# Performance work log

Hardware: AMD Instinct MI355X
Metric: run time of the kernel (lower is better)

## Reference

```python
import jax, jax.numpy as jnp
import numpy as np

B, S, D, H = 16, 512, 768, 12
DH = D // H


def setup_inputs() -> dict:
    key = jax.random.key(0)
    ks = jax.random.split(key, 12)
    hidden_states = jax.random.normal(ks[0], (B, S, D), dtype=jnp.float32)
    # additive padding mask: 0 for valid, -10000 for padded tail tokens
    lengths = jax.random.randint(ks[1], (B,), S // 2, S + 1)
    pad = (jnp.arange(S)[None, :] >= lengths[:, None]).astype(jnp.float32)
    attention_mask = (pad * -10000.0)[:, None, None, :]  # [B,1,1,S]
    # row-stochastic graph prior over codes
    pr = jax.random.uniform(ks[2], (B, S, S), dtype=jnp.float32)
    prior = pr / jnp.sum(pr, axis=-1, keepdims=True)
    s = 0.02
    params = dict(
        Wq=jax.random.normal(ks[3], (D, D)) * s, bq=jnp.zeros((D,)),
        Wk=jax.random.normal(ks[4], (D, D)) * s, bk=jnp.zeros((D,)),
        Wv=jax.random.normal(ks[5], (D, D)) * s, bv=jnp.zeros((D,)),
        Wg=jax.random.normal(ks[6], (D, 2)) * s, bg=jnp.zeros((2,)),
        Wo=jax.random.normal(ks[7], (D, D)) * s, bo=jnp.zeros((D,)),
        gamma=jnp.ones((D,)), beta=jnp.zeros((D,)),
    )
    return dict(hidden_states=hidden_states, attention_mask=attention_mask,
                prior=prior, **params)


def _layer_norm(x, gamma, beta, eps=1e-5):
    mu = jnp.mean(x, axis=-1, keepdims=True)
    var = jnp.mean(jnp.square(x - mu), axis=-1, keepdims=True)
    return (x - mu) * jax.lax.rsqrt(var + eps) * gamma + beta


def reference(hidden_states, attention_mask, prior,
              Wq, bq, Wk, bk, Wv, bv, Wg, bg, Wo, bo, gamma, beta):
    b, s, d = hidden_states.shape
    # project and split heads: [B,S,H,DH]
    q = (hidden_states @ Wq + bq).reshape(b, s, H, DH)
    k = (hidden_states @ Wk + bk).reshape(b, s, H, DH)
    v = (hidden_states @ Wv + bv).reshape(b, s, H, DH)
    scores = jnp.einsum('bshd,bthd->bhst', q, k) / jnp.sqrt(jnp.float32(DH))
    scores = scores + attention_mask  # broadcast [B,1,1,S]
    probs = jax.nn.softmax(scores, axis=-1)  # [B,H,S,S]
    # gate: avg-pool over valid tokens, softmax(linear/2)
    valid = (attention_mask.squeeze((1, 2)) == 0.0).astype(hidden_states.dtype)  # [B,S]
    denom = jnp.maximum(jnp.sum(valid, axis=1, keepdims=True), 1.0)
    h_pool = jnp.sum(hidden_states * valid[:, :, None], axis=1) / denom  # [B,D]
    gate = jax.nn.softmax((h_pool @ Wg + bg) / 2.0, axis=-1)  # [B,2]
    probs = probs * gate[:, 0, None, None, None] + prior[:, None, :, :] * gate[:, 1, None, None, None]
    ctx = jnp.einsum('bhst,bthd->bshd', probs, v).reshape(b, s, d)
    out = jax.nn.relu(ctx @ Wo + bo)
    out = _layer_norm(out + hidden_states, gamma, beta)
    return out
```

## Files before the change

kernel.cpp:

```cpp
#include <hip/hip_runtime.h>

#define NB_ 16
#define S_ 512
#define D_ 768
#define H_ 12
#define DH_ 64
#define QT_ 64
#define KT_ 128
#define LDQ_ 1536

typedef __attribute__((ext_vector_type(8))) short bf16x8;
typedef __attribute__((ext_vector_type(4))) float f32x4;
typedef unsigned short ushort_t;

__device__ __forceinline__ unsigned short f2bf(float f){
  unsigned int u = __float_as_uint(f);
  u += 0x7fffu + ((u >> 16) & 1u);
  return (unsigned short)(u >> 16);
}
__device__ __forceinline__ float bf2f(unsigned short s){
  return __uint_as_float(((unsigned int)s) << 16);
}
__device__ __forceinline__ unsigned int pack2(float a, float b){
  return (unsigned int)f2bf(a) | ((unsigned int)f2bf(b) << 16);
}
__device__ __forceinline__ void gld16(const ushort_t* g, ushort_t* l){
  __builtin_amdgcn_global_load_lds((const __attribute__((address_space(1))) unsigned int*)g,
                                   (__attribute__((address_space(3))) unsigned int*)l, 16, 0, 0);
}

__global__ __launch_bounds__(256) void k_setup(
    const float* __restrict__ hs, const float* __restrict__ mask, const float* __restrict__ prior,
    const float* __restrict__ W0, const float* __restrict__ W1,
    const float* __restrict__ W2, const float* __restrict__ W3,
    const float* __restrict__ b0, const float* __restrict__ b1, const float* __restrict__ b2,
    ushort_t* __restrict__ hsb, ushort_t* __restrict__ wt, float* __restrict__ bqkv,
    float* __restrict__ partial, float* __restrict__ pcnt, ushort_t* __restrict__ priorb)
{
  __shared__ float t[32][33];
  const int bx = blockIdx.x, tid = threadIdx.x;
  if (bx < 512){
    int chunk = bx & 31, b = bx >> 5;
    const float* mrow = mask + b * S_ + chunk * 16;
    const float* base = hs + ((size_t)b * S_ + chunk * 16) * D_;
    ushort_t* obase = hsb + ((size_t)b * S_ + chunk * 16) * D_;
    float a0 = 0.f, a1 = 0.f, a2 = 0.f, cnt = 0.f;
#pragma unroll 2
    for (int s = 0; s < 16; s++){
      const float* r = base + (size_t)s * D_;
      float x0 = r[tid], x1 = r[tid + 256], x2 = r[tid + 512];
      ushort_t* o = obase + (size_t)s * D_;
      o[tid] = f2bf(x0); o[tid + 256] = f2bf(x1); o[tid + 512] = f2bf(x2);
      if (mrow[s] == 0.0f){ a0 += x0; a1 += x1; a2 += x2; cnt += 1.0f; }
    }
    float* o = partial + (size_t)(b * 32 + chunk) * D_;
    o[tid] = a0; o[tid + 256] = a1; o[tid + 512] = a2;
    if (tid == 0) pcnt[b * 32 + chunk] = cnt;
  } else if (bx < 512 + 2304){
    int idx = bx - 512;
    int z = idx / 576, rem = idx - z * 576;
    int ky = rem / 24, nx = rem - ky * 24;
    const float* W = (z == 0) ? W0 : (z == 1) ? W1 : (z == 2) ? W2 : W3;
    ushort_t* o = wt + (size_t)z * D_ * D_;
    int j = tid & 31, i0 = tid >> 5;
    int kb = ky * 32, nb = nx * 32;
#pragma unroll
    for (int r = 0; r < 4; r++){
      int i = i0 + r * 8;
      t[i][j] = W[(size_t)(kb + i) * D_ + nb + j];
    }
    __syncthreads();
#pragma unroll
    for (int r = 0; r < 4; r++){
      int i = i0 + r * 8;
      o[(size_t)(nb + i) * D_ + kb + j] = f2bf(t[j][i]);
    }
  } else if (bx < 2825){
    int i = (bx - 2816) * 256 + tid;
    if (i < 3 * D_){
      float v = (i < D_) ? b0[i] : (i < 2 * D_) ? b1[i - D_] : b2[i - 2 * D_];
      bqkv[i] = v;
    }
  } else {
    size_t i = (size_t)(bx - 2825) * 4096 + (size_t)tid * 16;
    const float4* s4 = (const float4*)(prior + i);
    float4 f0 = s4[0], f1 = s4[1], f2 = s4[2], f3 = s4[3];
    uint4 p0, p1;
    p0.x = pack2(f0.x, f0.y); p0.y = pack2(f0.z, f0.w);
    p0.z = pack2(f1.x, f1.y); p0.w = pack2(f1.z, f1.w);
    p1.x = pack2(f2.x, f2.y); p1.y = pack2(f2.z, f2.w);
    p1.z = pack2(f3.x, f3.y); p1.w = pack2(f3.z, f3.w);
    *(uint4*)(priorb + i) = p0;
    *(uint4*)(priorb + i + 8) = p1;
  }
}

__global__ __launch_bounds__(256) void k_pool2(const float* __restrict__ partial, const float* __restrict__ pcnt,
                                               const float* __restrict__ Wg, const float* __restrict__ bg,
                                               float* __restrict__ gate){
  int b = blockIdx.x, tid = threadIdx.x;
  __shared__ float red[256];
  __shared__ float hp[768];
  float a0 = 0.f, a1 = 0.f, a2 = 0.f;
#pragma unroll
  for (int c = 0; c < 32; c++){
    const float* p = partial + (size_t)(b * 32 + c) * D_;
    a0 += p[tid]; a1 += p[tid + 256]; a2 += p[tid + 512];
  }
  float denom = 0.f;
#pragma unroll
  for (int c = 0; c < 32; c++) denom += pcnt[b * 32 + c];
  float inv = 1.0f / fmaxf(denom, 1.0f);
  hp[tid] = a0 * inv; hp[tid + 256] = a1 * inv; hp[tid + 512] = a2 * inv;
  __syncthreads();
  float p0 = 0.f, p1 = 0.f;
  for (int d = tid; d < D_; d += 256){ p0 += hp[d] * Wg[d * 2]; p1 += hp[d] * Wg[d * 2 + 1]; }
  red[tid] = p0; __syncthreads();
  for (int o = 128; o > 0; o >>= 1){ if (tid < o) red[tid] += red[tid + o]; __syncthreads(); }
  float z0 = red[0]; __syncthreads();
  red[tid] = p1; __syncthreads();
  for (int o = 128; o > 0; o >>= 1){ if (tid < o) red[tid] += red[tid + o]; __syncthreads(); }
  float z1 = red[0];
  if (tid == 0){
    z0 = (z0 + bg[0]) * 0.5f; z1 = (z1 + bg[1]) * 0.5f;
    float m = fmaxf(z0, z1);
    float e0 = __expf(z0 - m), e1 = __expf(z1 - m);
    float ssum = e0 + e1;
    gate[b * 2] = e0 / ssum; gate[b * 2 + 1] = e1 / ssum;
  }
}

template<int OUTBF16, int RELU, int RESID, int MAP, int VSPLIT>
__global__ __launch_bounds__(256, 2) void k_gemm_bt(
    const ushort_t* __restrict__ Am, long sA, int lda,
    const ushort_t* __restrict__ Bm, long sB, int ldb,
    void* __restrict__ Cp, long sC, int ldc, void* __restrict__ Cp2,
    const float* __restrict__ bias,
    const float* __restrict__ resid, float alpha, int K)
{
  __shared__ ushort_t As[2][128 * 64];
  __shared__ ushort_t Bs[2][128 * 64];
  int z, bm, bn;
  if (MAP == 2){ z = blockIdx.x; bm = blockIdx.y; bn = blockIdx.z; }
  else if (MAP == 1){ z = blockIdx.z; bm = blockIdx.x; bn = blockIdx.y; }
  else { z = blockIdx.z; bm = blockIdx.y; bn = blockIdx.x; }
  const ushort_t* Ab = Am + (size_t)z * sA;
  const ushort_t* Bb = Bm + (size_t)z * sB;
  const long coff = (long)z * sC;
  const int tid = threadIdx.x;
  const int m0 = bm * 128, n0 = bn * 128;
  const int wid = tid >> 6, lane = tid & 63;
  const int quad = lane >> 4, l16 = lane & 15;
  const int wm = wid >> 1, wn = wid & 1;
  const int sw = l16 & 7;

  auto stage = [&](int buf, int k0){
#pragma unroll
    for (int c = 0; c < 4; c++){
      int idx = tid + c * 256;
      int row = idx >> 3, p = idx & 7;
      int cg = p ^ (row & 7);
      gld16(Ab + (size_t)(m0 + row) * lda + k0 + cg * 8, &As[buf][idx * 8]);
    }
#pragma unroll
    for (int c = 0; c < 4; c++){
      int idx = tid + c * 256;
      int row = idx >> 3, p = idx & 7;
      int cg = p ^ (row & 7);
      gld16(Bb + (size_t)(n0 + row) * ldb + k0 + cg * 8, &Bs[buf][idx * 8]);
    }
  };

  f32x4 acc[4][4];
#pragma unroll
  for (int i = 0; i < 4; i++)
#pragma unroll
    for (int j = 0; j < 4; j++) acc[i][j] = (f32x4){0.f, 0.f, 0.f, 0.f};

  stage(0, 0);
  int cur = 0;
  for (int k0 = 0; k0 < K; k0 += 64){
    if (k0 + 64 < K){
      stage(cur ^ 1, k0 + 64);
      __builtin_amdgcn_sched_barrier(0);
      asm volatile("s_waitcnt vmcnt(8)" ::: "memory");
    } else {
      __builtin_amdgcn_sched_barrier(0);
      asm volatile("s_waitcnt vmcnt(0)" ::: "memory");
    }
    __builtin_amdgcn_sched_barrier(0);
    __builtin_amdgcn_s_barrier();
#pragma unroll
    for (int ks = 0; ks < 2; ks++){
      bf16x8 af[4], bfv[4];
#pragma unroll
      for (int mi = 0; mi < 4; mi++){
        int row = wm * 64 + mi * 16 + l16;
        af[mi] = *(const bf16x8*)(&As[cur][(row * 8 + ((ks * 4 + quad) ^ sw)) * 8]);
      }
#pragma unroll
      for (int ni = 0; ni < 4; ni++){
        int row = wn * 64 + ni * 16 + l16;
        bfv[ni] = *(const bf16x8*)(&Bs[cur][(row * 8 + ((ks * 4 + quad) ^ sw)) * 8]);
      }
      __builtin_amdgcn_s_setprio(1);
#pragma unroll
      for (int mi = 0; mi < 4; mi++)
#pragma unroll
        for (int ni = 0; ni < 4; ni++)
          acc[mi][ni] = __builtin_amdgcn_mfma_f32_16x16x32_bf16(af[mi], bfv[ni], acc[mi][ni], 0, 0, 0);
      __builtin_amdgcn_s_setprio(0);
    }
    __builtin_amdgcn_sched_barrier(0);
    __builtin_amdgcn_s_barrier();
    cur ^= 1;
  }

  if (VSPLIT && n0 >= 1536){
    ushort_t* vtp = (ushort_t*)Cp2;
    const int bb = m0 >> 9;
#pragma unroll
    for (int mi = 0; mi < 4; mi++){
#pragma unroll
      for (int ni = 0; ni < 4; ni++){
        int col = n0 + wn * 64 + ni * 16 + l16;
        float bcol = bias[col];
        int hh = (col - 1536) >> 6, dh = (col - 1536) & 63;
        int trow = (m0 & 511) + wm * 64 + mi * 16 + quad * 4;
        uint2 pk;
        pk.x = pack2(acc[mi][ni][0] + bcol, acc[mi][ni][1] + bcol);
        pk.y = pack2(acc[mi][ni][2] + bcol, acc[mi][ni][3] + bcol);
        *(uint2*)(vtp + ((size_t)(bb * H_ + hh) * DH_ + dh) * S_ + trow) = pk;
      }
    }
    return;
  }

#pragma unroll
  for (int mi = 0; mi < 4; mi++){
#pragma unroll
    for (int ni = 0; ni < 4; ni++){
      int col = n0 + wn * 64 + ni * 16 + l16;
      float bcol = bias ? bias[col] : 0.0f;
#pragma unroll
      for (int r = 0; r < 4; r++){
        int row = m0 + wm * 64 + mi * 16 + quad * 4 + r;
        float v = acc[mi][ni][r] * alpha + bcol;
        if (RELU) v = fmaxf(v, 0.0f);
        if (RESID) v += resid[(size_t)row * ldc + col];
        long idx = coff + (long)row * ldc + col;
        if (OUTBF16) ((ushort_t*)Cp)[idx] = f2bf(v);
        else         ((float*)Cp)[idx] = v;
      }
    }
  }
}

__global__ __launch_bounds__(512, 2) void k_gemm8_qkv(
    const ushort_t* __restrict__ A,
    const ushort_t* __restrict__ B,
    ushort_t* __restrict__ Cq,
    ushort_t* __restrict__ vt,
    const float* __restrict__ bias)
{
  __shared__ ushort_t Al[2][2][256 * 32];
  __shared__ ushort_t Bl[2][2][256 * 32];
  const int tid = threadIdx.x;
  const int m0 = blockIdx.x * 256, n0 = blockIdx.y * 256;
  const int wid = tid >> 6, lane = tid & 63;
  const int quad = lane >> 4, l16 = lane & 15;
  const int wm = wid >> 2, wn = wid & 3;

  const int i0c = tid, i1c = tid + 512;
  const int r0 = i0c >> 2, c0 = (i0c & 3) ^ (r0 & 3);
  const int r1 = i1c >> 2, c1 = (i1c & 3) ^ (r1 & 3);
  const size_t a0 = (size_t)(m0 + r0) * 768 + c0 * 8;
  const size_t a1 = (size_t)(m0 + r1) * 768 + c1 * 8;
  const size_t b0 = (size_t)(n0 + r0) * 768 + c0 * 8;
  const size_t b1 = (size_t)(n0 + r1) * 768 + c1 * 8;

  auto stA = [&](int slot, int ks, int kt){
    int ko = kt * 64 + ks * 32;
    gld16(A + a0 + ko, &Al[slot][ks][i0c * 8]);
    gld16(A + a1 + ko, &Al[slot][ks][i1c * 8]);
  };
  auto stB = [&](int slot, int ks, int kt){
    int ko = kt * 64 + ks * 32;
    gld16(B + b0 + ko, &Bl[slot][ks][i0c * 8]);
    gld16(B + b1 + ko, &Bl[slot][ks][i1c * 8]);
  };
  auto rdA = [&](int slot, int ks, int mi) -> bf16x8 {
    int row = wm * 128 + mi * 16 + l16;
    return *(const bf16x8*)(&Al[slot][ks][(row * 4 + (quad ^ (row & 3))) * 8]);
  };
  auto rdB = [&](int slot, int ks, int ni) -> bf16x8 {
    int row = wn * 64 + ni * 16 + l16;
    return *(const bf16x8*)(&Bl[slot][ks][(row * 4 + (quad ^ (row & 3))) * 8]);
  };

  f32x4 acc[8][4];
#pragma unroll
  for (int i = 0; i < 8; i++)
#pragma unroll
    for (int j = 0; j < 4; j++) acc[i][j] = (f32x4){0.f, 0.f, 0.f, 0.f};

  stA(0, 0, 0); stB(0, 0, 0); stA(0, 1, 0); stB(0, 1, 0);
  stA(1, 0, 1); stB(1, 0, 1); stA(1, 1, 1);
  __builtin_amdgcn_sched_barrier(0);
  asm volatile("s_waitcnt vmcnt(6)" ::: "memory");
  __builtin_amdgcn_sched_barrier(0);
  __builtin_amdgcn_s_barrier();

#pragma unroll 2
  for (int t = 0; t < 12; ++t){
    const int s = t & 1, o = s ^ 1;
    bf16x8 aL[8], aH[8], bL[4], bH[4];
#pragma unroll
    for (int mi = 0; mi < 8; mi++) aL[mi] = rdA(s, 0, mi);
#pragma unroll
    for (int ni = 0; ni < 4; ni++) bL[ni] = rdB(s, 0, ni);
    if (t + 1 < 12) stB(o, 1, t + 1);
    __builtin_amdgcn_sched_barrier(0);
    __builtin_amdgcn_s_barrier();
    asm volatile("s_waitcnt lgkmcnt(0)" ::: "memory");
    __builtin_amdgcn_sched_barrier(0);
    __builtin_amdgcn_s_setprio(1);
#pragma unroll
    for (int mi = 0; mi < 4; mi++)
#pragma unroll
      for (int ni = 0; ni < 4; ni++)
        acc[mi][ni] = __builtin_amdgcn_mfma_f32_16x16x32_bf16(aL[mi], bL[ni], acc[mi][ni], 0, 0, 0);
    __builtin_amdgcn_s_setprio(0);
    __builtin_amdgcn_sched_barrier(0);
    __builtin_amdgcn_s_barrier();
#pragma unroll
    for (int ni = 0; ni < 4; ni++) bH[ni] = rdB(s, 1, ni);
    if (t + 2 < 12) stA(s, 0, t + 2);
    __builtin_amdgcn_sched_barrier(0);
    __builtin_amdgcn_s_barrier();
    asm volatile("s_waitcnt lgkmcnt(0)" ::: "memory");
    __builtin_amdgcn_sched_barrier(0);
    __builtin_amdgcn_s_setprio(1);
#pragma unroll
    for (int mi = 4; mi < 8; mi++)
#pragma unroll
      for (int ni = 0; ni < 4; ni++)
        acc[mi][ni] = __builtin_amdgcn_mfma_f32_16x16x32_bf16(aL[mi], bL[ni], acc[mi][ni], 0, 0, 0);
    __builtin_amdgcn_s_setprio(0);
    __builtin_amdgcn_sched_barrier(0);
    __builtin_amdgcn_s_barrier();
#pragma unroll
    for (int mi = 0; mi < 8; mi++) aH[mi] = rdA(s, 1, mi);
    if (t + 2 < 12) stB(s, 0, t + 2);
    __builtin_amdgcn_sched_barrier(0);
    __builtin_amdgcn_s_barrier();
    asm volatile("s_waitcnt lgkmcnt(0)" ::: "memory");
    __builtin_amdgcn_sched_barrier(0);
    __builtin_amdgcn_s_setprio(1);
#pragma unroll
    for (int mi = 0; mi < 4; mi++)
#pragma unroll
      for (int ni = 0; ni < 4; ni++)
        acc[mi][ni] = __builtin_amdgcn_mfma_f32_16x16x32_bf16(aH[mi], bH[ni], acc[mi][ni], 0, 0, 0);
    __builtin_amdgcn_s_setprio(0);
    __builtin_amdgcn_sched_barrier(0);
    __builtin_amdgcn_s_barrier();
    if (t + 2 < 12) stA(s, 1, t + 2);
    __builtin_amdgcn_sched_barrier(0);
    __builtin_amdgcn_s_barrier();
    __builtin_amdgcn_s_setprio(1);
#pragma unroll
    for (int mi = 4; mi < 8; mi++)
#pragma unroll
      for (int ni = 0; ni < 4; ni++)
        acc[mi][ni] = __builtin_amdgcn_mfma_f32_16x16x32_bf16(aH[mi], bH[ni], acc[mi][ni], 0, 0, 0);
    __builtin_amdgcn_s_setprio(0);
    __builtin_amdgcn_sched_barrier(0);
    if (t < 10) { asm volatile("s_waitcnt vmcnt(6)" ::: "memory"); }
    else        { asm volatile("s_waitcnt vmcnt(0)" ::: "memory"); }
    __builtin_amdgcn_sched_barrier(0);
    __builtin_amdgcn_s_barrier();
  }

  if (n0 >= 1536){
    const int bb = m0 >> 9;
#pragma unroll
    for (int mi = 0; mi < 8; mi++){
#pragma unroll
      for (int ni = 0; ni < 4; ni++){
        int col = n0 + wn * 64 + ni * 16 + l16;
        float bcol = bias[col];
        int hh = (col - 1536) >> 6, dh = (col - 1536) & 63;
        int trow = (m0 & 511) + wm * 128 + mi * 16 + quad * 4;
        uint2 pk;
        pk.x = pack2(acc[mi][ni][0] + bcol, acc[mi][ni][1] + bcol);
        pk.y = pack2(acc[mi][ni][2] + bcol, acc[mi][ni][3] + bcol);
        *(uint2*)(vt + ((size_t)(bb * H_ + hh) * DH_ + dh) * S_ + trow) = pk;
      }
    }
    return;
  }
#pragma unroll
  for (int mi = 0; mi < 8; mi++){
#pragma unroll
    for (int ni = 0; ni < 4; ni++){
      int col = n0 + wn * 64 + ni * 16 + l16;
      float bcol = bias[col];
#pragma unroll
      for (int r = 0; r < 4; r++){
        int row = m0 + wm * 128 + mi * 16 + quad * 4 + r;
        Cq[(size_t)row * LDQ_ + col] = f2bf(acc[mi][ni][r] + bcol);
      }
    }
  }
}

__global__ __launch_bounds__(256) void k_flash(
    const ushort_t* __restrict__ qkv,
    const ushort_t* __restrict__ vt,
    const ushort_t* __restrict__ priorctx,
    const float* __restrict__ mask,
    const float* __restrict__ gate,
    ushort_t* __restrict__ ctx)
{
  __shared__ ushort_t Ks[KT_ * 64];
  __shared__ ushort_t Vs[DH_ * 128];
  __shared__ ushort_t Ps[QT_ * 136];
  __shared__ float rs[QT_];
  const int z = blockIdx.x, b = z / H_, h = z - b * H_;
  const int q0 = blockIdx.y * QT_;
  const int tid = threadIdx.x;
  const int wid = tid >> 6, lane = tid & 63, quad = lane >> 4, l16 = lane & 15;

  bf16x8 bq[4][2];
#pragma unroll
  for (int ni = 0; ni < 4; ni++)
#pragma unroll
    for (int ks = 0; ks < 2; ks++)
      bq[ni][ks] = *(const bf16x8*)(qkv + ((size_t)(b * S_ + q0 + ni * 16 + l16)) * LDQ_
                                    + h * DH_ + ks * 32 + quad * 8);
  if (tid < QT_) rs[tid] = 0.f;

  f32x4 accv[4];
#pragma unroll
  for (int ni = 0; ni < 4; ni++) accv[ni] = (f32x4){0.f, 0.f, 0.f, 0.f};

  for (int t0 = 0; t0 < S_; t0 += KT_){
    if (mask[b * S_ + t0] != 0.0f) break;
#pragma unroll
    for (int c = 0; c < 4; c++){
      int idx = tid + c * 256;
      int row = idx >> 3, p = idx & 7;
      int cg = p ^ (row & 7);
      gld16(qkv + ((size_t)(b * S_ + t0 + row)) * LDQ_ + D_ + h * DH_ + cg * 8, &Ks[idx * 8]);
    }
#pragma unroll
    for (int c = 0; c < 4; c++){
      int idx = tid + c * 256;
      int row = idx >> 4, p = idx & 15;
      int cg = p ^ (row & 15);
      gld16(vt + (size_t)z * (DH_ * S_) + (size_t)row * S_ + t0 + cg * 8, &Vs[idx * 8]);
    }
    __syncthreads();

    f32x4 accs[2][4];
#pragma unroll
    for (int mi = 0; mi < 2; mi++)
#pragma unroll
      for (int ni = 0; ni < 4; ni++) accs[mi][ni] = (f32x4){0.f, 0.f, 0.f, 0.f};
#pragma unroll
    for (int ks = 0; ks < 2; ks++){
      bf16x8 ak[2];
#pragma unroll
      for (int mi = 0; mi < 2; mi++){
        int row = wid * 32 + mi * 16 + l16;
        ak[mi] = *(const bf16x8*)(&Ks[(row * 8 + ((ks * 4 + quad) ^ (l16 & 7))) * 8]);
      }
#pragma unroll
      for (int mi = 0; mi < 2; mi++)
#pragma unroll
        for (int ni = 0; ni < 4; ni++)
          accs[mi][ni] = __builtin_amdgcn_mfma_f32_16x16x32_bf16(ak[mi], bq[ni][ks], accs[mi][ni], 0, 0, 0);
    }

    float mv[2][4];
#pragma unroll
    for (int mi = 0; mi < 2; mi++)
#pragma unroll
      for (int r = 0; r < 4; r++)
        mv[mi][r] = mask[b * S_ + t0 + wid * 32 + mi * 16 + quad * 4 + r];
    float rowpart[4] = {0.f, 0.f, 0.f, 0.f};
#pragma unroll
    for (int mi = 0; mi < 2; mi++){
#pragma unroll
      for (int ni = 0; ni < 4; ni++){
        float e0 = __expf(accs[mi][ni][0] * 0.125f + mv[mi][0]);
        float e1 = __expf(accs[mi][ni][1] * 0.125f + mv[mi][1]);
        float e2 = __expf(accs[mi][ni][2] * 0.125f + mv[mi][2]);
        float e3 = __expf(accs[mi][ni][3] * 0.125f + mv[mi][3]);
        rowpart[ni] += (e0 + e1) + (e2 + e3);
        uint2 pk;
        pk.x = pack2(e0, e1);
        pk.y = pack2(e2, e3);
        *(uint2*)(&Ps[(ni * 16 + l16) * 136 + wid * 32 + mi * 16 + quad * 4]) = pk;
      }
    }
#pragma unroll
    for (int ni = 0; ni < 4; ni++){
      rowpart[ni] += __shfl_xor(rowpart[ni], 16);
      rowpart[ni] += __shfl_xor(rowpart[ni], 32);
    }
    if (lane < 16){
#pragma unroll
      for (int ni = 0; ni < 4; ni++) atomicAdd(&rs[ni * 16 + l16], rowpart[ni]);
    }
    __syncthreads();

#pragma unroll
    for (int ks = 0; ks < 4; ks++){
      bf16x8 ap = *(const bf16x8*)(&Ps[(wid * 16 + l16) * 136 + ks * 32 + quad * 8]);
#pragma unroll
      for (int ni = 0; ni < 4; ni++){
        bf16x8 bv8 = *(const bf16x8*)(&Vs[((ni * 16 + l16) * 16 + ((ks * 4 + quad) ^ l16)) * 8]);
        accv[ni] = __builtin_amdgcn_mfma_f32_16x16x32_bf16(ap, bv8, accv[ni], 0, 0, 0);
      }
    }
    __syncthreads();
  }

  const float g0 = gate[b * 2], g1 = gate[b * 2 + 1];
#pragma unroll
  for (int ni = 0; ni < 4; ni++){
#pragma unroll
    for (int r = 0; r < 4; r++){
      int q = wid * 16 + quad * 4 + r;
      int dh = ni * 16 + l16;
      float scl = g0 / rs[q];
      size_t idx = ((size_t)(b * S_ + q0 + q)) * D_ + h * DH_ + dh;
      float v = accv[ni][r] * scl + g1 * bf2f(priorctx[idx]);
      ctx[idx] = f2bf(v);
    }
  }
}

__global__ __launch_bounds__(256) void k_ln(float* __restrict__ out, const float* __restrict__ gamma,
                                            const float* __restrict__ beta){
  __shared__ float red[256];
  int row = blockIdx.x, tid = threadIdx.x;
  float* p = out + (size_t)row * D_;
  float x0 = p[tid], x1 = p[tid + 256], x2 = p[tid + 512];
  red[tid] = x0 + x1 + x2; __syncthreads();
  for (int o = 128; o > 0; o >>= 1){ if (tid < o) red[tid] += red[tid + o]; __syncthreads(); }
  float mu = red[0] * (1.0f / 768.0f);
  __syncthreads();
  float d0 = x0 - mu, d1 = x1 - mu, d2 = x2 - mu;
  red[tid] = d0 * d0 + d1 * d1 + d2 * d2; __syncthreads();
  for (int o = 128; o > 0; o >>= 1){ if (tid < o) red[tid] += red[tid + o]; __syncthreads(); }
  float rsv = rsqrtf(red[0] * (1.0f / 768.0f) + 1e-5f);
  p[tid]       = d0 * rsv * gamma[tid]       + beta[tid];
  p[tid + 256] = d1 * rsv * gamma[tid + 256] + beta[tid + 256];
  p[tid + 512] = d2 * rsv * gamma[tid + 512] + beta[tid + 512];
}

extern "C" void kernel_launch(void* const* d_in, const int* in_sizes, int n_in,
                              void* d_out, int out_size, void* d_ws, size_t ws_size,
                              hipStream_t stream){
  const float* hs    = (const float*)d_in[0];
  const float* mask  = (const float*)d_in[1];
  const float* prior = (const float*)d_in[2];
  const float* Wq = (const float*)d_in[3];  const float* bq = (const float*)d_in[4];
  const float* Wk = (const float*)d_in[5];  const float* bk = (const float*)d_in[6];
  const float* Wv = (const float*)d_in[7];  const float* bv = (const float*)d_in[8];
  const float* Wg = (const float*)d_in[9];  const float* bg = (const float*)d_in[10];
  const float* Wo = (const float*)d_in[11]; const float* bo = (const float*)d_in[12];
  const float* gamma = (const float*)d_in[13]; const float* beta = (const float*)d_in[14];
  float* out = (float*)d_out;

  size_t off = 0;
  auto alloc = [&](size_t bytes) -> char* {
    char* p = (char*)d_ws + off;
    off += (bytes + 255) & ~(size_t)255;
    return p;
  };
  const size_t HSD = (size_t)NB_ * S_ * D_;
  ushort_t* hsb     = (ushort_t*)alloc(HSD * 2);
  ushort_t* qkvb    = (ushort_t*)alloc(HSD * 2 * 2);
  ushort_t* vtb     = (ushort_t*)alloc(HSD * 2);
  ushort_t* wt      = (ushort_t*)alloc((size_t)4 * D_ * D_ * 2);
  ushort_t* priorctx= (ushort_t*)alloc(HSD * 2);
  ushort_t* ctx     = (ushort_t*)alloc(HSD * 2);
  float*    bqkv    = (float*)alloc((size_t)3 * D_ * 4);
  float*    gate    = (float*)alloc(256);
  float*    partial = (float*)alloc((size_t)NB_ * 32 * D_ * 4);
  float*    pcnt    = (float*)alloc((size_t)NB_ * 32 * 4);
  ushort_t* priorb  = ctx;

  k_setup<<<dim3(3849), 256, 0, stream>>>(hs, mask, prior, Wq, Wk, Wv, Wo, bq, bk, bv,
                                          hsb, wt, bqkv, partial, pcnt, priorb);
  k_pool2<<<dim3(NB_), 256, 0, stream>>>(partial, pcnt, Wg, bg, gate);
  k_gemm8_qkv<<<dim3(32, 9), 512, 0, stream>>>(hsb, wt, qkvb, vtb, bqkv);
  k_gemm_bt<1, 0, 0, 2, 0><<<dim3(16, 4, 6), 256, 0, stream>>>(
      priorb, (long)S_ * S_, S_, vtb, (long)H_ * DH_ * S_, S_,
      priorctx, (long)S_ * D_, D_, nullptr, nullptr, nullptr, 1.0f, S_);
  k_flash<<<dim3(NB_ * H_, S_ / QT_), 256, 0, stream>>>(
      qkvb, vtb, priorctx, mask, gate, ctx);
  k_gemm_bt<0, 1, 1, 1, 0><<<dim3(64, 6, 1), 256, 0, stream>>>(
      ctx, 0, D_, wt + 3 * (size_t)D_ * D_, 0, D_, out, 0, D_, nullptr, bo, hs, 1.0f, D_);
  k_ln<<<dim3(NB_ * S_), 256, 0, stream>>>(out, gamma, beta);
}
```

Before: 274.4 us.

## Restructure QKV GEMM shared tiles into 128-row halves with 8-chunk XOR swizzle

Changes the LDS layout of the QKV GEMM from K-split halves (256 rows x 32 cols) to row-split halves (128 rows x 64 cols) with an 8-way XOR swizzle. Each warp now reads from a single row-half, and global loads fetch 128-byte contiguous row segments instead of 64-byte ones. The prefetch order and the vmcnt waits are reworked to match: B halves are loaded one step ahead into the other slot, and A halves two steps ahead into the current slot. This aims to improve global-load coalescing and reduce LDS bank conflicts, at the risk of a more fragile overlap and wait schedule.

```diff
diff --git a/kernel.cpp b/kernel.cpp
--- a/kernel.cpp
+++ b/kernel.cpp
@@ -263,39 +263,36 @@
     ushort_t* __restrict__ vt,
     const float* __restrict__ bias)
 {
-  __shared__ ushort_t Al[2][2][256 * 32];
-  __shared__ ushort_t Bl[2][2][256 * 32];
+  __shared__ ushort_t Al[2][2][128 * 64];
+  __shared__ ushort_t Bl[2][2][128 * 64];
   const int tid = threadIdx.x;
   const int m0 = blockIdx.x * 256, n0 = blockIdx.y * 256;
   const int wid = tid >> 6, lane = tid & 63;
   const int quad = lane >> 4, l16 = lane & 15;
   const int wm = wid >> 2, wn = wid & 3;
+  const int sw = l16 & 7;
 
   const int i0c = tid, i1c = tid + 512;
-  const int r0 = i0c >> 2, c0 = (i0c & 3) ^ (r0 & 3);
-  const int r1 = i1c >> 2, c1 = (i1c & 3) ^ (r1 & 3);
-  const size_t a0 = (size_t)(m0 + r0) * 768 + c0 * 8;
-  const size_t a1 = (size_t)(m0 + r1) * 768 + c1 * 8;
-  const size_t b0 = (size_t)(n0 + r0) * 768 + c0 * 8;
-  const size_t b1 = (size_t)(n0 + r1) * 768 + c1 * 8;
-
-  auto stA = [&](int slot, int ks, int kt){
-    int ko = kt * 64 + ks * 32;
-    gld16(A + a0 + ko, &Al[slot][ks][i0c * 8]);
-    gld16(A + a1 + ko, &Al[slot][ks][i1c * 8]);
+  const int r0 = i0c >> 3, c0 = (i0c & 7) ^ (r0 & 7);
+  const int r1 = i1c >> 3, c1 = (i1c & 7) ^ (r1 & 7);
+
+  auto stA = [&](int slot, int h, int kt){
+    const ushort_t* src = A + (size_t)(m0 + h * 128) * 768 + kt * 64;
+    gld16(src + (size_t)r0 * 768 + c0 * 8, &Al[slot][h][i0c * 8]);
+    gld16(src + (size_t)r1 * 768 + c1 * 8, &Al[slot][h][i1c * 8]);
   };
-  auto stB = [&](int slot, int ks, int kt){
-    int ko = kt * 64 + ks * 32;
-    gld16(B + b0 + ko, &Bl[slot][ks][i0c * 8]);
-    gld16(B + b1 + ko, &Bl[slot][ks][i1c * 8]);
+  auto stB = [&](int slot, int h, int kt){
+    const ushort_t* src = B + (size_t)(n0 + h * 128) * 768 + kt * 64;
+    gld16(src + (size_t)r0 * 768 + c0 * 8, &Bl[slot][h][i0c * 8]);
+    gld16(src + (size_t)r1 * 768 + c1 * 8, &Bl[slot][h][i1c * 8]);
   };
   auto rdA = [&](int slot, int ks, int mi) -> bf16x8 {
-    int row = wm * 128 + mi * 16 + l16;
-    return *(const bf16x8*)(&Al[slot][ks][(row * 4 + (quad ^ (row & 3))) * 8]);
+    int rr = mi * 16 + l16;
+    return *(const bf16x8*)(&Al[slot][wm][(rr * 8 + ((ks * 4 + quad) ^ sw)) * 8]);
   };
   auto rdB = [&](int slot, int ks, int ni) -> bf16x8 {
-    int row = wn * 64 + ni * 16 + l16;
-    return *(const bf16x8*)(&Bl[slot][ks][(row * 4 + (quad ^ (row & 3))) * 8]);
+    int rr = (wn & 1) * 64 + ni * 16 + l16;
+    return *(const bf16x8*)(&Bl[slot][wn >> 1][(rr * 8 + ((ks * 4 + quad) ^ sw)) * 8]);
   };
 
   f32x4 acc[8][4];
@@ -304,10 +301,10 @@
 #pragma unroll
     for (int j = 0; j < 4; j++) acc[i][j] = (f32x4){0.f, 0.f, 0.f, 0.f};
 
-  stA(0, 0, 0); stB(0, 0, 0); stA(0, 1, 0); stB(0, 1, 0);
-  stA(1, 0, 1); stB(1, 0, 1); stA(1, 1, 1);
+  stA(0, 0, 0); stA(0, 1, 0); stB(0, 0, 0); stB(0, 1, 0);
+  stA(1, 0, 1); stA(1, 1, 1);
   __builtin_amdgcn_sched_barrier(0);
-  asm volatile("s_waitcnt vmcnt(6)" ::: "memory");
+  asm volatile("s_waitcnt vmcnt(4)" ::: "memory");
   __builtin_amdgcn_sched_barrier(0);
   __builtin_amdgcn_s_barrier();
 
@@ -319,7 +316,7 @@
     for (int mi = 0; mi < 8; mi++) aL[mi] = rdA(s, 0, mi);
 #pragma unroll
     for (int ni = 0; ni < 4; ni++) bL[ni] = rdB(s, 0, ni);
-    if (t + 1 < 12) stB(o, 1, t + 1);
+    if (t + 1 < 12) stB(o, 0, t + 1);
     __builtin_amdgcn_sched_barrier(0);
     __builtin_amdgcn_s_barrier();
     asm volatile("s_waitcnt lgkmcnt(0)" ::: "memory");
@@ -334,8 +331,8 @@
     __builtin_amdgcn_sched_barrier(0);
     __builtin_amdgcn_s_barrier();
 #pragma unroll
-    for (int ni = 0; ni < 4; ni++) bH[ni] = rdB(s, 1, ni);
-    if (t + 2 < 12) stA(s, 0, t + 2);
+    for (int mi = 0; mi < 8; mi++) aH[mi] = rdA(s, 1, mi);
+    if (t + 1 < 12) stB(o, 1, t + 1);
     __builtin_amdgcn_sched_barrier(0);
     __builtin_amdgcn_s_barrier();
     asm volatile("s_waitcnt lgkmcnt(0)" ::: "memory");
@@ -350,8 +347,8 @@
     __builtin_amdgcn_sched_barrier(0);
     __builtin_amdgcn_s_barrier();
 #pragma unroll
-    for (int mi = 0; mi < 8; mi++) aH[mi] = rdA(s, 1, mi);
-    if (t + 2 < 12) stB(s, 0, t + 2);
+    for (int ni = 0; ni < 4; ni++) bH[ni] = rdB(s, 1, ni);
+    if (t + 2 < 12) stA(s, 0, t + 2);
     __builtin_amdgcn_sched_barrier(0);
     __builtin_amdgcn_s_barrier();
     asm volatile("s_waitcnt lgkmcnt(0)" ::: "memory");
@@ -376,8 +373,8 @@
         acc[mi][ni] = __builtin_amdgcn_mfma_f32_16x16x32_bf16(aH[mi], bH[ni], acc[mi][ni], 0, 0, 0);
     __builtin_amdgcn_s_setprio(0);
     __builtin_amdgcn_sched_barrier(0);
-    if (t < 10) { asm volatile("s_waitcnt vmcnt(6)" ::: "memory"); }
-    else        { asm volatile("s_waitcnt vmcnt(0)" ::: "memory"); }
+    if (t <= 9)       { asm volatile("s_waitcnt vmcnt(4)" ::: "memory"); }
+    else if (t == 10) { asm volatile("s_waitcnt vmcnt(0)" ::: "memory"); }
     __builtin_amdgcn_sched_barrier(0);
     __builtin_amdgcn_s_barrier();
   }
```

Result: no change. 276.7 us (+0.8%).
